# Performance work log

Hardware: AMD Instinct MI355X
Metric: run time of the kernel (lower is better)

The kernel has to match this reference:

```python
import jax, jax.numpy as jnp
from jax import lax
import numpy as np

S = 3600  # spatial_size from scn.InputLayer
B = 1     # batch
P = 200000
NEG = jnp.float32(-1e30)


def setup_inputs() -> dict:
    key = jax.random.key(0)
    ks = jax.random.split(key, 10)
    coords = jax.random.randint(ks[0], (P, 2), 0, S, dtype=jnp.int32)
    features = jax.random.normal(ks[1], (P, 1), jnp.float32)
    w1 = jax.random.normal(ks[2], (5, 5, 1, 10), jnp.float32) * 0.2
    w2 = jax.random.normal(ks[3], (5, 5, 10, 64), jnp.float32) * 0.06
    w3 = jax.random.normal(ks[4], (5, 5, 64, 128), jnp.float32) * 0.025
    w4 = jax.random.normal(ks[5], (5, 5, 128, 256), jnp.float32) * 0.018
    fc1_w = jax.random.normal(ks[6], (256 * 9 * 9, 32), jnp.float32) * 0.01
    fc1_b = jax.random.normal(ks[7], (32,), jnp.float32) * 0.01
    fc2_w = jax.random.normal(ks[8], (32, 5), jnp.float32) * 0.1
    fc2_b = jax.random.normal(ks[9], (5,), jnp.float32) * 0.01
    return dict(coords=coords, features=features, w1=w1, w2=w2, w3=w3, w4=w4,
                fc1_w=fc1_w, fc1_b=fc1_b, fc2_w=fc2_w, fc2_b=fc2_b)


def _subm_conv(x, mask, w):
    # Submanifold conv == dense SAME conv on zero-filled grid, output kept
    # only at active sites (inactive inputs are exactly zero by construction).
    y = lax.conv_general_dilated(x, w, (1, 1), 'SAME',
                                 dimension_numbers=('NHWC', 'HWIO', 'NHWC'))
    return y * mask


def _sparse_maxpool(x, mask, k):
    # scn.MaxPooling: max over ACTIVE sites in each window; output site is
    # active iff any input site in the window is active, else feature = 0.
    neg = jnp.where(mask > 0, x, NEG)
    y = lax.reduce_window(neg, NEG, lax.max, (1, k, k, 1), (1, k, k, 1), 'VALID')
    new_mask = lax.reduce_window(mask, jnp.float32(0), lax.max,
                                 (1, k, k, 1), (1, k, k, 1), 'VALID')
    return jnp.where(new_mask > 0, y, 0.0), new_mask


def reference(coords, features, w1, w2, w3, w4, fc1_w, fc1_b, fc2_w, fc2_b):
    # scn.InputLayer: scatter sparse (coord, feature) pairs onto the grid
    x = jnp.zeros((B, S, S, 1), jnp.float32).at[0, coords[:, 0], coords[:, 1], :].add(features)
    mask = jnp.zeros((B, S, S, 1), jnp.float32).at[0, coords[:, 0], coords[:, 1], :].set(1.0)

    x = jax.nn.elu(_subm_conv(x, mask, w1))
    x, mask = _sparse_maxpool(x, mask, 5)   # 3600 -> 720
    x = jax.nn.elu(_subm_conv(x, mask, w2))
    x, mask = _sparse_maxpool(x, mask, 5)   # 720 -> 144
    x = jax.nn.elu(_subm_conv(x, mask, w3))
    x, mask = _sparse_maxpool(x, mask, 4)   # 144 -> 36
    x = jax.nn.elu(_subm_conv(x, mask, w4))
    x, mask = _sparse_maxpool(x, mask, 4)   # 36 -> 9

    # SparseToDense -> (B, 256, 9, 9), then view(-1, 256*9*9) in NCHW order
    h = x.transpose(0, 3, 1, 2).reshape(B, 256 * 9 * 9)
    h = jax.nn.elu(h @ fc1_w + fc1_b)
    logits = h @ fc2_w + fc2_b
    return jax.nn.softmax(logits, axis=1)
```

## Files before the change

### kernel.cpp

```cpp
#include <hip/hip_runtime.h>
#include <math.h>

#define S0 3600
#define S1 720
#define S2 144
#define S3 36
#define S4 9
#define NEGF (-1e30f)

static constexpr size_t OFF_X0  = 0;
static constexpr size_t OFF_M0B = (size_t)S0 * S0 * 4;
static constexpr size_t OFF_Y1  = OFF_M0B + 1620000;
static constexpr size_t OFF_M1  = OFF_Y1 + (size_t)S1 * S1 * 10 * 4;
static constexpr size_t OFF_M2  = 1330000;
static constexpr size_t OFF_Y3  = OFF_M2 + 20736;
static constexpr size_t OFF_M3  = OFF_Y3 + (size_t)S3 * S3 * 128 * 4;
static constexpr size_t OFF_Y4  = OFF_M3 + 1296;
static constexpr size_t OFF_H1  = OFF_Y4 + (size_t)S4 * S4 * 256 * 4;
static constexpr size_t OFF_Y2H = 13000000;
static constexpr size_t OFF_W3H = 18400000;
static constexpr size_t OFF_W2H = 19240000;
static constexpr size_t OFF_W4H = 19400000;

typedef __attribute__((ext_vector_type(8))) short bf16x8;
typedef __attribute__((ext_vector_type(4))) float f32x4;

__device__ __forceinline__ float eluf(float x) { return x > 0.f ? x : expm1f(x); }
__device__ __forceinline__ unsigned short f2bf(float f) {
    unsigned u = __float_as_uint(f);
    unsigned r = u + 0x7FFFu + ((u >> 16) & 1u);
    return (unsigned short)(r >> 16);
}
__device__ __forceinline__ float bf2f(unsigned short h) {
    return __uint_as_float((unsigned)h << 16);
}

__global__ __launch_bounds__(256) void k_zero(const int* __restrict__ coords,
                                              float* __restrict__ x0, int P) {
    int i = blockIdx.x * 256 + threadIdx.x;
    if (i >= P) return;
    x0[coords[2 * i] * S0 + coords[2 * i + 1]] = 0.f;
}

__global__ __launch_bounds__(256) void k_scatter(const int* __restrict__ coords,
                                                 const float* __restrict__ feats,
                                                 float* __restrict__ x0,
                                                 unsigned* __restrict__ m0b, int P) {
    int i = blockIdx.x * 256 + threadIdx.x;
    if (i >= P) return;
    int r = coords[2 * i], c = coords[2 * i + 1];
    int idx = r * S0 + c;
    atomicAdd(&x0[idx], feats[i]);
    atomicOr(&m0b[idx >> 5], 1u << (idx & 31));
}

__global__ __launch_bounds__(256) void k_l1(const float* __restrict__ x0,
                                            const unsigned* __restrict__ m0b,
                                            const float* __restrict__ w1,
                                            float* __restrict__ y1,
                                            unsigned char* __restrict__ m1) {
    __shared__ float w1s[250];
    int tid = threadIdx.x;
    if (tid < 250) w1s[tid] = w1[tid];
    __syncthreads();
    int t = blockIdx.x * 256 + tid;
    int pr = t / S1, pc = t % S1;
    int r0 = pr * 5 - 2, c0 = pc * 5 - 2;
    unsigned rows[9];
#pragma unroll
    for (int rr = 0; rr < 9; rr++) {
        unsigned bits = 0;
        int gr = r0 + rr;
        if (gr >= 0 && gr < S0) {
            int cs = c0 < 0 ? 0 : c0;
            int ce = c0 + 8 > S0 - 1 ? S0 - 1 : c0 + 8;
            int span = ce - cs;
            size_t i0 = (size_t)gr * S0 + cs;
            unsigned sh = (unsigned)(i0 & 31);
            unsigned long long two = (unsigned long long)m0b[i0 >> 5] >> sh;
            if ((int)sh + span >= 32)
                two |= (unsigned long long)m0b[(i0 >> 5) + 1] << (32 - sh);
            bits = (unsigned)(two & ((1u << (span + 1)) - 1));
            bits <<= (cs - c0);
        }
        rows[rr] = bits;
    }
    unsigned any25 = 0;
#pragma unroll
    for (int dy = 0; dy < 5; dy++) any25 |= (rows[2 + dy] >> 2) & 0x1Fu;
    float* yo = &y1[(size_t)t * 10];
    if (!any25) {
#pragma unroll
        for (int q = 0; q < 5; q++) ((float2*)yo)[q] = make_float2(0.f, 0.f);
        m1[t] = 0;
        return;
    }
    float2 mx[5];
#pragma unroll
    for (int q = 0; q < 5; q++) mx[q] = make_float2(NEGF, NEGF);
    for (int dy = 0; dy < 5; dy++) {
        unsigned crow = (rows[2 + dy] >> 2) & 0x1Fu;
        while (crow) {
            int dx = __ffs(crow) - 1; crow &= crow - 1;
            float2 acc[5];
#pragma unroll
            for (int q = 0; q < 5; q++) acc[q] = make_float2(0.f, 0.f);
#pragma unroll
            for (int ky = 0; ky < 5; ky++) {
                unsigned nrow = (rows[dy + ky] >> dx) & 0x1Fu;
                size_t rowbase = (size_t)(r0 + dy + ky) * S0 + (c0 + dx);
                while (nrow) {
                    int kx = __ffs(nrow) - 1; nrow &= nrow - 1;
                    float xv = x0[rowbase + kx];
                    const float2* wp = (const float2*)&w1s[(ky * 5 + kx) * 10];
#pragma unroll
                    for (int q = 0; q < 5; q++) {
                        float2 w = wp[q];
                        acc[q].x = fmaf(xv, w.x, acc[q].x);
                        acc[q].y = fmaf(xv, w.y, acc[q].y);
                    }
                }
            }
#pragma unroll
            for (int q = 0; q < 5; q++) {
                mx[q].x = fmaxf(mx[q].x, acc[q].x);
                mx[q].y = fmaxf(mx[q].y, acc[q].y);
            }
        }
    }
#pragma unroll
    for (int q = 0; q < 5; q++) {
        float2 o;
        o.x = eluf(mx[q].x); o.y = eluf(mx[q].y);
        ((float2*)yo)[q] = o;
    }
    m1[t] = 1;
}

__global__ __launch_bounds__(256) void k_cvtw_all(const float* __restrict__ w2,
                                                  const float* __restrict__ w3,
                                                  const float* __restrict__ w4,
                                                  unsigned short* __restrict__ w2h,
                                                  unsigned short* __restrict__ w3h,
                                                  unsigned short* __restrict__ w4h) {
    int blk = blockIdx.x;
    int tid = threadIdx.x;
    if (blk < 13) {
        int t = blk * 256 + tid;
        int s = t >> 8, rem = t & 255;
        int nt = rem >> 6, lane = rem & 63;
        int quad = lane >> 4, n = lane & 15;
        int tap = 2 * s + (quad >> 1);
#pragma unroll
        for (int j = 0; j < 8; j++) {
            int ci = (quad & 1) * 8 + j;
            float v = 0.f;
            if (tap < 25 && ci < 10) v = w2[(tap * 10 + ci) * 64 + nt * 16 + n];
            w2h[(size_t)t * 8 + j] = f2bf(v);
        }
    } else if (blk < 113) {
        int t = (blk - 13) * 256 + tid;
        int s = t >> 9, rem = t & 511;
        int nt = rem >> 6, lane = rem & 63;
        int quad = lane >> 4, n = lane & 15;
        int t5 = s >> 1, cib = s & 1;
#pragma unroll
        for (int j = 0; j < 8; j++) {
            int ci = cib * 32 + quad * 8 + j;
            float v = w3[(size_t)(t5 * 64 + ci) * 128 + nt * 16 + n];
            w3h[(size_t)t * 8 + j] = f2bf(v);
        }
    } else {
        int t = (blk - 113) * 256 + tid;
        int s = t >> 10, rem = t & 1023;
        int nt = rem >> 6, lane = rem & 63;
        int quad = lane >> 4, n = lane & 15;
        int t5 = s >> 2, cib = s & 3;
#pragma unroll
        for (int j = 0; j < 8; j++) {
            int ci = cib * 32 + quad * 8 + j;
            float v = w4[(size_t)(t5 * 128 + ci) * 256 + nt * 16 + n];
            w4h[(size_t)t * 8 + j] = f2bf(v);
        }
    }
}

__global__ __launch_bounds__(256, 4) void k_l2(const float* __restrict__ y1,
                                               const unsigned char* __restrict__ m1,
                                               const unsigned short* __restrict__ w2h,
                                               unsigned short* __restrict__ y2h,
                                               unsigned char* __restrict__ m2) {
    __shared__ unsigned short winh[240 * 16];
    __shared__ unsigned char sm[196];
    int b = blockIdx.x;
    int bpr = b / 72, bpc = b % 72;
    int r0 = bpr * 10 - 2, c0 = bpc * 10 - 2;
    int tid = threadIdx.x;
    if (tid < 240) {
        unsigned uh[8] = {0, 0, 0, 0, 0, 0, 0, 0};
        if (tid < 196) {
            int gr = r0 + tid / 14, gc = c0 + tid % 14;
            bool ok = (gr >= 0 && gr < S1 && gc >= 0 && gc < S1);
            sm[tid] = ok ? m1[gr * S1 + gc] : (unsigned char)0;
            if (ok) {
                const float2* src = (const float2*)&y1[(size_t)(gr * S1 + gc) * 10];
#pragma unroll
                for (int q = 0; q < 5; q++) {
                    float2 v = src[q];
                    unsigned short h0 = f2bf(v.x), h1 = f2bf(v.y);
                    uh[q] = (unsigned)h0 | ((unsigned)h1 << 16);
                }
            }
        }
        uint4* dh = (uint4*)&winh[tid * 16];
        dh[0] = make_uint4(uh[0], uh[1], uh[2], uh[3]);
        dh[1] = make_uint4(uh[4], uh[5], uh[6], uh[7]);
    }
    __syncthreads();
    int wv = tid >> 6;
    int a = wv >> 1, bq = wv & 1;
    int lane = tid & 63, quad = lane >> 4, n = lane & 15;
    int cql = lane & 31, s01l = lane >> 5;
    bool pv = false;
    if (cql < 25)
        pv = sm[(a * 5 + 2 + cql / 5) * 14 + s01l * 5 + 2 + cql % 5] != 0;
    unsigned long long bal = __ballot(pv);
    unsigned mb[2];
    mb[0] = (unsigned)(bal & 0x1FFFFFFull);
    mb[1] = (unsigned)((bal >> 32) & 0x1FFFFFFull);
    const bf16x8* wh8 = (const bf16x8*)w2h;
    const bf16x8* xh8 = (const bf16x8*)winh;
    int oct = quad & 1, qh = quad >> 1;
    int base[2][2];
#pragma unroll
    for (int s01 = 0; s01 < 2; s01++)
#pragma unroll
        for (int mt = 0; mt < 2; mt++) {
            int cell = mt * 16 + n;
            base[s01][mt] = ((a * 5 + cell / 5) * 14 + s01 * 5 + cell % 5) * 2 + oct;
        }
    constexpr int TOFF[26] = {0, 1, 2, 3, 4, 14, 15, 16, 17, 18, 28, 29, 30, 31,
                              32, 42, 43, 44, 45, 46, 56, 57, 58, 59, 60, 70};
    f32x4 acc[2][2][2];
#pragma unroll
    for (int s01 = 0; s01 < 2; s01++)
#pragma unroll
        for (int mt = 0; mt < 2; mt++)
#pragma unroll
            for (int ntl = 0; ntl < 2; ntl++) acc[s01][mt][ntl] = (f32x4){0.f, 0.f, 0.f, 0.f};
#pragma unroll
    for (int s = 0; s < 13; s++) {
        int toff2 = 2 * (qh ? TOFF[2 * s + 1] : TOFF[2 * s]);
        bf16x8 ah[2][2];
#pragma unroll
        for (int s01 = 0; s01 < 2; s01++)
#pragma unroll
            for (int mt = 0; mt < 2; mt++) ah[s01][mt] = xh8[base[s01][mt] + toff2];
#pragma unroll
        for (int ntl = 0; ntl < 2; ntl++) {
            bf16x8 bh = wh8[(s * 4 + bq * 2 + ntl) * 64 + lane];
#pragma unroll
            for (int s01 = 0; s01 < 2; s01++)
#pragma unroll
                for (int mt = 0; mt < 2; mt++)
                    acc[s01][mt][ntl] = __builtin_amdgcn_mfma_f32_16x16x32_bf16(ah[s01][mt], bh, acc[s01][mt][ntl], 0, 0, 0);
        }
    }
#pragma unroll
    for (int s01 = 0; s01 < 2; s01++) {
        int gsite = (bpr * 2 + a) * S2 + bpc * 2 + s01;
#pragma unroll
        for (int ntl = 0; ntl < 2; ntl++) {
            float m = NEGF;
#pragma unroll
            for (int mt = 0; mt < 2; mt++) {
#pragma unroll
                for (int r = 0; r < 4; r++) {
                    int cell = mt * 16 + quad * 4 + r;
                    if (cell < 25 && (mb[s01] & (1u << cell))) m = fmaxf(m, acc[s01][mt][ntl][r]);
                }
            }
            m = fmaxf(m, __shfl_xor(m, 16, 64));
            m = fmaxf(m, __shfl_xor(m, 32, 64));
            if (quad == 0) {
                int nt = bq * 2 + ntl;
                y2h[(size_t)gsite * 64 + nt * 16 + n] = mb[s01] ? f2bf(eluf(m)) : (unsigned short)0;
            }
        }
        if (bq == 0 && lane == 0) m2[gsite] = mb[s01] ? 1 : 0;
    }
}

__global__ __launch_bounds__(256) void k_l3(const unsigned short* __restrict__ y2h,
                                            const unsigned char* __restrict__ m2,
                                            const unsigned short* __restrict__ w3h,
                                            float* __restrict__ y3,
                                            unsigned char* __restrict__ m3) {
    __shared__ uint4 win_h4[1152];
    __shared__ unsigned char sm[64];
    int b = blockIdx.x;
    int pr2 = b / 18, pc2 = b % 18;
    int r0 = pr2 * 8 - 2, c0 = pc2 * 8 - 2;
    int tid = threadIdx.x;
    for (int k = tid; k < 1152; k += 256) {
        int cellk = k >> 3, q = k & 7;
        int gr = r0 + cellk / 12, gc = c0 + cellk % 12;
        uint4 vh = make_uint4(0, 0, 0, 0);
        if (gr >= 0 && gr < S2 && gc >= 0 && gc < S2)
            vh = ((const uint4*)y2h)[(size_t)(gr * S2 + gc) * 8 + q];
        win_h4[k] = vh;
    }
    if (tid < 64) sm[tid] = m2[(pr2 * 8 + (tid >> 3)) * S2 + pc2 * 8 + (tid & 7)];
    __syncthreads();
    const bf16x8* winh8 = (const bf16x8*)win_h4;
    const bf16x8* w3h8 = (const bf16x8*)w3h;
    int wv = tid >> 6, lane = tid & 63;
    int quad = lane >> 4, n = lane & 15;
    int cellr = n >> 2, cellc = n & 3;
    f32x4 acc[4][2];
#pragma unroll
    for (int si = 0; si < 4; si++)
#pragma unroll
        for (int ntl = 0; ntl < 2; ntl++) acc[si][ntl] = (f32x4){0.f, 0.f, 0.f, 0.f};
    int bb = (wv * 2) * 64 + lane;
    bf16x8 bh0 = w3h8[bb];
    bf16x8 bh1 = w3h8[bb + 64];
#pragma unroll 2
    for (int s = 0; s < 50; s++) {
        int sp = s + 1 < 50 ? s + 1 : 0;
        int nb = (sp * 8 + wv * 2) * 64 + lane;
        bf16x8 nh0 = w3h8[nb];
        bf16x8 nh1 = w3h8[nb + 64];
        int t5 = s >> 1, cib = s & 1;
        int ky = t5 / 5, kx = t5 % 5;
        int common = ((cellr + ky) * 12 + (cellc + kx)) * 8 + cib * 4 + quad;
#pragma unroll
        for (int si = 0; si < 4; si++) {
            bf16x8 ah = winh8[common + (si >> 1) * 384 + (si & 1) * 32];
            acc[si][0] = __builtin_amdgcn_mfma_f32_16x16x32_bf16(ah, bh0, acc[si][0], 0, 0, 0);
            acc[si][1] = __builtin_amdgcn_mfma_f32_16x16x32_bf16(ah, bh1, acc[si][1], 0, 0, 0);
        }
        bh0 = nh0; bh1 = nh1;
    }
#pragma unroll
    for (int si = 0; si < 4; si++) {
        int srb = (si >> 1) * 4, scb = (si & 1) * 4;
        bool anyv = false;
#pragma unroll
        for (int i = 0; i < 16; i++) anyv |= (sm[(srb + (i >> 2)) * 8 + scb + (i & 3)] != 0);
        int sg = (2 * pr2 + (si >> 1)) * S3 + 2 * pc2 + (si & 1);
#pragma unroll
        for (int ntl = 0; ntl < 2; ntl++) {
            float mv = NEGF;
#pragma unroll
            for (int r = 0; r < 4; r++) {
                int cell = quad * 4 + r;
                if (sm[(srb + (cell >> 2)) * 8 + scb + (cell & 3)]) mv = fmaxf(mv, acc[si][ntl][r]);
            }
            mv = fmaxf(mv, __shfl_xor(mv, 16, 64));
            mv = fmaxf(mv, __shfl_xor(mv, 32, 64));
            if (quad == 0)
                y3[(size_t)sg * 128 + (wv * 2 + ntl) * 16 + n] = anyv ? eluf(mv) : 0.f;
        }
        if (tid == 0) m3[sg] = anyv ? 1 : 0;
    }
}

__global__ __launch_bounds__(1024) void k_l4(const float* __restrict__ y3,
                                             const unsigned char* __restrict__ m3,
                                             const unsigned short* __restrict__ w4h,
                                             float* __restrict__ y4) {
    __shared__ unsigned short winh[64 * 128];
    __shared__ unsigned char sm[16];
    int p = blockIdx.x;
    int ppr = p / S4, ppc = p % S4;
    int r0 = ppr * 4 - 2, c0 = ppc * 4 - 2;
    int tid = threadIdx.x;
    for (int k = tid; k < 2048; k += 1024) {
        int cellk = k >> 5, q = k & 31;
        int gr = r0 + (cellk >> 3), gc = c0 + (cellk & 7);
        float4 v = make_float4(0.f, 0.f, 0.f, 0.f);
        if (gr >= 0 && gr < S3 && gc >= 0 && gc < S3)
            v = ((const float4*)y3)[((size_t)gr * S3 + gc) * 32 + q];
        unsigned short h0 = f2bf(v.x), h1 = f2bf(v.y), h2 = f2bf(v.z), h3 = f2bf(v.w);
        unsigned uh0 = (unsigned)h0 | ((unsigned)h1 << 16);
        unsigned uh1 = (unsigned)h2 | ((unsigned)h3 << 16);
        ((uint2*)winh)[k] = make_uint2(uh0, uh1);
    }
    if (tid < 16) sm[tid] = m3[(ppr * 4 + (tid >> 2)) * S3 + ppc * 4 + (tid & 3)];
    __syncthreads();
    const bf16x8* winh8 = (const bf16x8*)winh;
    const bf16x8* w4h8 = (const bf16x8*)w4h;
    int wv = tid >> 6, lane = tid & 63;
    int quad = lane >> 4, n = lane & 15;
    int cellr = n >> 2, cellc = n & 3;
    f32x4 acc = {0.f, 0.f, 0.f, 0.f};
    int wb = wv * 64 + lane;
    bf16x8 bha = w4h8[wb];
    bf16x8 bhb = w4h8[1024 + wb];
#pragma unroll 2
    for (int s = 0; s < 100; s++) {
        int sp = s + 2 < 100 ? s + 2 : 0;
        bf16x8 nh = w4h8[sp * 1024 + wb];
        int t5 = s >> 2, cib = s & 3;
        int ky = t5 / 5, kx = t5 % 5;
        int aidx = ((cellr + ky) * 8 + (cellc + kx)) * 16 + cib * 4 + quad;
        bf16x8 ah = winh8[aidx];
        acc = __builtin_amdgcn_mfma_f32_16x16x32_bf16(ah, bha, acc, 0, 0, 0);
        bha = bhb; bhb = nh;
    }
    bool anyv = false;
#pragma unroll
    for (int i = 0; i < 16; i++) anyv |= (sm[i] != 0);
    float m = NEGF;
#pragma unroll
    for (int r = 0; r < 4; r++) {
        int cell = quad * 4 + r;
        if (sm[cell]) m = fmaxf(m, acc[r]);
    }
    m = fmaxf(m, __shfl_xor(m, 16, 64));
    m = fmaxf(m, __shfl_xor(m, 32, 64));
    if (quad == 0)
        y4[(size_t)p * 256 + wv * 16 + n] = anyv ? eluf(m) : 0.f;
}

__global__ __launch_bounds__(256) void k_fc1(const float* __restrict__ y4,
                                             const float* __restrict__ fc1_w,
                                             float* __restrict__ h1) {
    __shared__ float wsum[4][32];
    int t = threadIdx.x;
    int i = blockIdx.x * 256 + t;
    int c = i / 81, rem = i % 81;
    float x = y4[(size_t)rem * 256 + c];
    const float4* wr = (const float4*)&fc1_w[(size_t)i * 32];
    float4 w[8];
#pragma unroll
    for (int q = 0; q < 8; q++) w[q] = wr[q];
    int lane = t & 63, wv = t >> 6;
#pragma unroll
    for (int q = 0; q < 8; q++) {
#pragma unroll
        for (int k = 0; k < 4; k++) {
            float v = x * ((&w[q].x)[k]);
            v += __shfl_down(v, 32, 64);
            v += __shfl_down(v, 16, 64);
            v += __shfl_down(v, 8, 64);
            v += __shfl_down(v, 4, 64);
            v += __shfl_down(v, 2, 64);
            v += __shfl_down(v, 1, 64);
            if (lane == 0) wsum[wv][q * 4 + k] = v;
        }
    }
    __syncthreads();
    if (t < 32) {
        float s = wsum[0][t] + wsum[1][t] + wsum[2][t] + wsum[3][t];
        atomicAdd(&h1[t], s);
    }
}

__global__ __launch_bounds__(64) void k_fc2(const float* __restrict__ h1,
                                            const float* __restrict__ fc1_b,
                                            const float* __restrict__ fc2_w,
                                            const float* __restrict__ fc2_b,
                                            float* __restrict__ out) {
    __shared__ float hv[32];
    __shared__ float lg[5];
    int tid = threadIdx.x;
    if (tid < 32) hv[tid] = eluf(h1[tid] + fc1_b[tid]);
    __syncthreads();
    if (tid < 5) {
        float s = fc2_b[tid];
        for (int j = 0; j < 32; j++) s = fmaf(hv[j], fc2_w[j * 5 + tid], s);
        lg[tid] = s;
    }
    __syncthreads();
    if (tid == 0) {
        float m = lg[0];
        for (int k = 1; k < 5; k++) m = fmaxf(m, lg[k]);
        float e[5], sum = 0.f;
        for (int k = 0; k < 5; k++) { e[k] = expf(lg[k] - m); sum += e[k]; }
        for (int k = 0; k < 5; k++) out[k] = e[k] / sum;
    }
}

extern "C" void kernel_launch(void* const* d_in, const int* in_sizes, int n_in,
                              void* d_out, int out_size, void* d_ws, size_t ws_size,
                              hipStream_t stream) {
    const int* coords = (const int*)d_in[0];
    const float* feats = (const float*)d_in[1];
    const float* w1 = (const float*)d_in[2];
    const float* w2 = (const float*)d_in[3];
    const float* w3 = (const float*)d_in[4];
    const float* w4 = (const float*)d_in[5];
    const float* fc1w = (const float*)d_in[6];
    const float* fc1b = (const float*)d_in[7];
    const float* fc2w = (const float*)d_in[8];
    const float* fc2b = (const float*)d_in[9];
    float* out = (float*)d_out;
    char* ws = (char*)d_ws;
    float* x0 = (float*)(ws + OFF_X0);
    unsigned* m0b = (unsigned*)(ws + OFF_M0B);
    float* y1 = (float*)(ws + OFF_Y1);
    unsigned char* m1g = (unsigned char*)(ws + OFF_M1);
    unsigned char* m2g = (unsigned char*)(ws + OFF_M2);
    float* y3 = (float*)(ws + OFF_Y3);
    unsigned char* m3g = (unsigned char*)(ws + OFF_M3);
    float* y4 = (float*)(ws + OFF_Y4);
    float* h1 = (float*)(ws + OFF_H1);
    unsigned short* y2h = (unsigned short*)(ws + OFF_Y2H);
    unsigned short* w3h = (unsigned short*)(ws + OFF_W3H);
    unsigned short* w2h = (unsigned short*)(ws + OFF_W2H);
    unsigned short* w4h = (unsigned short*)(ws + OFF_W4H);
    int P = in_sizes[1];

    hipMemsetAsync(ws + OFF_M0B, 0, 1620000, stream);
    k_zero<<<(P + 255) / 256, 256, 0, stream>>>(coords, x0, P);
    k_scatter<<<(P + 255) / 256, 256, 0, stream>>>(coords, feats, x0, m0b, P);
    k_l1<<<(S1 * S1) / 256, 256, 0, stream>>>(x0, m0b, w1, y1, m1g);
    k_cvtw_all<<<513, 256, 0, stream>>>(w2, w3, w4, w2h, w3h, w4h);
    k_l2<<<72 * 72, 256, 0, stream>>>(y1, m1g, w2h, y2h, m2g);
    k_l3<<<18 * 18, 256, 0, stream>>>(y2h, m2g, w3h, y3, m3g);
    k_l4<<<S4 * S4, 1024, 0, stream>>>(y3, m3g, w4h, y4);
    hipMemsetAsync(ws + OFF_H1, 0, 128, stream);
    k_fc1<<<81, 256, 0, stream>>>(y4, fc1w, h1);
    k_fc2<<<1, 64, 0, stream>>>(h1, fc1b, fc2w, fc2b, out);
}
```

Before: 240.5 us.

## Store layer-1 output as padded bf16 and merge h1 memset into mask memset

Layer 1 now writes its activations directly as bf16, padded to 16 channels per site, so layer 2 can load each site with two 16-byte vector loads instead of five float2 loads plus conversion. This shrinks the intermediate buffer traffic from 40 to 32 bytes per site and takes the conversion work out of the layer-2 staging loop. The h1 accumulator is moved next to the mask bitmap so one memset clears both, removing a separate memset launch. Rounding behaviour is unchanged because layer 2 already converted these values to bf16.

```diff
diff --git a/kernel.cpp b/kernel.cpp
--- a/kernel.cpp
+++ b/kernel.cpp
@@ -10,13 +10,13 @@
 
 static constexpr size_t OFF_X0  = 0;
 static constexpr size_t OFF_M0B = (size_t)S0 * S0 * 4;
-static constexpr size_t OFF_Y1  = OFF_M0B + 1620000;
-static constexpr size_t OFF_M1  = OFF_Y1 + (size_t)S1 * S1 * 10 * 4;
+static constexpr size_t OFF_H1  = OFF_M0B + 1620000;
+static constexpr size_t OFF_Y1H = OFF_H1 + 128;
+static constexpr size_t OFF_M1  = OFF_Y1H + (size_t)S1 * S1 * 16 * 2;
 static constexpr size_t OFF_M2  = 1330000;
 static constexpr size_t OFF_Y3  = OFF_M2 + 20736;
 static constexpr size_t OFF_M3  = OFF_Y3 + (size_t)S3 * S3 * 128 * 4;
 static constexpr size_t OFF_Y4  = OFF_M3 + 1296;
-static constexpr size_t OFF_H1  = OFF_Y4 + (size_t)S4 * S4 * 256 * 4;
 static constexpr size_t OFF_Y2H = 13000000;
 static constexpr size_t OFF_W3H = 18400000;
 static constexpr size_t OFF_W2H = 19240000;
@@ -57,7 +57,7 @@
 __global__ __launch_bounds__(256) void k_l1(const float* __restrict__ x0,
                                             const unsigned* __restrict__ m0b,
                                             const float* __restrict__ w1,
-                                            float* __restrict__ y1,
+                                            unsigned short* __restrict__ y1h,
                                             unsigned char* __restrict__ m1) {
     __shared__ float w1s[250];
     int tid = threadIdx.x;
@@ -88,10 +88,10 @@
     unsigned any25 = 0;
 #pragma unroll
     for (int dy = 0; dy < 5; dy++) any25 |= (rows[2 + dy] >> 2) & 0x1Fu;
-    float* yo = &y1[(size_t)t * 10];
+    uint4* yo = (uint4*)&y1h[(size_t)t * 16];
     if (!any25) {
-#pragma unroll
-        for (int q = 0; q < 5; q++) ((float2*)yo)[q] = make_float2(0.f, 0.f);
+        yo[0] = make_uint4(0, 0, 0, 0);
+        yo[1] = make_uint4(0, 0, 0, 0);
         m1[t] = 0;
         return;
     }
@@ -128,12 +128,16 @@
             }
         }
     }
+    unsigned u[8];
 #pragma unroll
     for (int q = 0; q < 5; q++) {
-        float2 o;
-        o.x = eluf(mx[q].x); o.y = eluf(mx[q].y);
-        ((float2*)yo)[q] = o;
-    }
+        unsigned short h0 = f2bf(eluf(mx[q].x));
+        unsigned short h1 = f2bf(eluf(mx[q].y));
+        u[q] = (unsigned)h0 | ((unsigned)h1 << 16);
+    }
+    u[5] = 0; u[6] = 0; u[7] = 0;
+    yo[0] = make_uint4(u[0], u[1], u[2], u[3]);
+    yo[1] = make_uint4(u[4], u[5], u[6], u[7]);
     m1[t] = 1;
 }
 
@@ -185,7 +189,7 @@
     }
 }
 
-__global__ __launch_bounds__(256, 4) void k_l2(const float* __restrict__ y1,
+__global__ __launch_bounds__(256, 4) void k_l2(const unsigned short* __restrict__ y1h,
                                                const unsigned char* __restrict__ m1,
                                                const unsigned short* __restrict__ w2h,
                                                unsigned short* __restrict__ y2h,
@@ -197,24 +201,20 @@
     int r0 = bpr * 10 - 2, c0 = bpc * 10 - 2;
     int tid = threadIdx.x;
     if (tid < 240) {
-        unsigned uh[8] = {0, 0, 0, 0, 0, 0, 0, 0};
+        uint4 v0 = make_uint4(0, 0, 0, 0), v1 = v0;
         if (tid < 196) {
             int gr = r0 + tid / 14, gc = c0 + tid % 14;
             bool ok = (gr >= 0 && gr < S1 && gc >= 0 && gc < S1);
             sm[tid] = ok ? m1[gr * S1 + gc] : (unsigned char)0;
             if (ok) {
-                const float2* src = (const float2*)&y1[(size_t)(gr * S1 + gc) * 10];
-#pragma unroll
-                for (int q = 0; q < 5; q++) {
-                    float2 v = src[q];
-                    unsigned short h0 = f2bf(v.x), h1 = f2bf(v.y);
-                    uh[q] = (unsigned)h0 | ((unsigned)h1 << 16);
-                }
+                const uint4* src = (const uint4*)&y1h[(size_t)(gr * S1 + gc) * 16];
+                v0 = src[0];
+                v1 = src[1];
             }
         }
         uint4* dh = (uint4*)&winh[tid * 16];
-        dh[0] = make_uint4(uh[0], uh[1], uh[2], uh[3]);
-        dh[1] = make_uint4(uh[4], uh[5], uh[6], uh[7]);
+        dh[0] = v0;
+        dh[1] = v1;
     }
     __syncthreads();
     int wv = tid >> 6;
@@ -500,7 +500,7 @@
     char* ws = (char*)d_ws;
     float* x0 = (float*)(ws + OFF_X0);
     unsigned* m0b = (unsigned*)(ws + OFF_M0B);
-    float* y1 = (float*)(ws + OFF_Y1);
+    unsigned short* y1h = (unsigned short*)(ws + OFF_Y1H);
     unsigned char* m1g = (unsigned char*)(ws + OFF_M1);
     unsigned char* m2g = (unsigned char*)(ws + OFF_M2);
     float* y3 = (float*)(ws + OFF_Y3);
@@ -513,15 +513,14 @@
     unsigned short* w4h = (unsigned short*)(ws + OFF_W4H);
     int P = in_sizes[1];
 
-    hipMemsetAsync(ws + OFF_M0B, 0, 1620000, stream);
+    hipMemsetAsync(ws + OFF_M0B, 0, 1620000 + 128, stream);
     k_zero<<<(P + 255) / 256, 256, 0, stream>>>(coords, x0, P);
     k_scatter<<<(P + 255) / 256, 256, 0, stream>>>(coords, feats, x0, m0b, P);
-    k_l1<<<(S1 * S1) / 256, 256, 0, stream>>>(x0, m0b, w1, y1, m1g);
+    k_l1<<<(S1 * S1) / 256, 256, 0, stream>>>(x0, m0b, w1, y1h, m1g);
     k_cvtw_all<<<513, 256, 0, stream>>>(w2, w3, w4, w2h, w3h, w4h);
-    k_l2<<<72 * 72, 256, 0, stream>>>(y1, m1g, w2h, y2h, m2g);
+    k_l2<<<72 * 72, 256, 0, stream>>>(y1h, m1g, w2h, y2h, m2g);
     k_l3<<<18 * 18, 256, 0, stream>>>(y2h, m2g, w3h, y3, m3g);
     k_l4<<<S4 * S4, 1024, 0, stream>>>(y3, m3g, w4h, y4);
-    hipMemsetAsync(ws + OFF_H1, 0, 128, stream);
     k_fc1<<<81, 256, 0, stream>>>(y4, fc1w, h1);
     k_fc2<<<1, 64, 0, stream>>>(h1, fc1b, fc2w, fc2b, out);
 }
```

Measured after the change: 235.7 us. 2.0% less time.
